# Kernel tuning notes

Hardware: AMD Instinct MI355X
Metric: run time of the kernel (lower is better)

## Reference

```python
import jax, jax.numpy as jnp
import numpy as np

D_MODEL = 2048
NUM_HEADS = 16
N_KV_HEADS = 4
HEAD_DIM = D_MODEL // NUM_HEADS  # 128
N_REP = NUM_HEADS // N_KV_HEADS  # 4
WINDOW = 256
ROPE_BASE = 10000.0
B, T = 2, 2048


def setup_inputs() -> dict:
    key = jax.random.key(0)
    ks = jax.random.split(key, 5)
    s_in = 1.0 / np.sqrt(D_MODEL)
    return {
        "x": jax.random.normal(ks[0], (B, T, D_MODEL), jnp.float32),
        "Wq": jax.random.normal(ks[1], (D_MODEL, D_MODEL), jnp.float32) * s_in,
        "Wk": jax.random.normal(ks[2], (D_MODEL, N_KV_HEADS * HEAD_DIM), jnp.float32) * s_in,
        "Wv": jax.random.normal(ks[3], (D_MODEL, N_KV_HEADS * HEAD_DIM), jnp.float32) * s_in,
        "Wo": jax.random.normal(ks[4], (D_MODEL, D_MODEL), jnp.float32) * s_in,
    }


def _rope_tables(seqlen, dtype):
    inv_freq = 1.0 / (ROPE_BASE ** (jnp.arange(0, HEAD_DIM, 2, dtype=jnp.float32) / HEAD_DIM))
    t = jnp.arange(seqlen, dtype=jnp.float32)
    freqs = jnp.outer(t, inv_freq)              # [T, hd/2]
    emb = jnp.concatenate([freqs, freqs], -1)   # [T, hd]
    return jnp.cos(emb).astype(dtype), jnp.sin(emb).astype(dtype)


def _rotate_half(x):
    half = x.shape[-1] // 2
    return jnp.concatenate([-x[..., half:], x[..., :half]], -1)


def reference(x, Wq, Wk, Wv, Wo):
    Bb, Tt, _ = x.shape
    q = (x @ Wq).reshape(Bb, Tt, NUM_HEADS, HEAD_DIM).transpose(0, 2, 1, 3)   # [B,H,T,hd]
    k = (x @ Wk).reshape(Bb, Tt, N_KV_HEADS, HEAD_DIM).transpose(0, 2, 1, 3)  # [B,Hkv,T,hd]
    v = (x @ Wv).reshape(Bb, Tt, N_KV_HEADS, HEAD_DIM).transpose(0, 2, 1, 3)

    cos, sin = _rope_tables(Tt, q.dtype)  # [T, hd] each, broadcast over B,H
    q = q * cos + _rotate_half(q) * sin
    k = k * cos + _rotate_half(k) * sin

    # GQA: repeat kv heads to match query heads
    k = jnp.repeat(k, N_REP, axis=1)
    v = jnp.repeat(v, N_REP, axis=1)

    # banded causal sliding-window mask: 0 <= i - j < WINDOW
    rel = jnp.arange(Tt)[:, None] - jnp.arange(Tt)[None, :]
    allowed = (rel >= 0) & (rel < WINDOW)  # [T, T]

    scale = 1.0 / np.sqrt(HEAD_DIM)
    scores = jnp.einsum('bhqd,bhkd->bhqk', q, k) * scale
    scores = jnp.where(allowed, scores, jnp.finfo(scores.dtype).min)
    probs = jax.nn.softmax(scores, axis=-1)
    y = jnp.einsum('bhqk,bhkd->bhqd', probs, v)
    y = y.transpose(0, 2, 1, 3).reshape(Bb, Tt, D_MODEL)
    return y @ Wo
```

## Files before the change

### kernel.cpp

```cpp
#include <hip/hip_runtime.h>
#include <hip/hip_bf16.h>

#define D_MODEL 2048
#define SEQ_T   2048
#define NQH     16
#define NKVH    4
#define HD      128
#define WIN     256
#define BATCH   2
#define ROWS    (BATCH * SEQ_T)
#define L2_10K  13.287712379549449f

typedef __attribute__((ext_vector_type(8))) short bf8_t;
typedef __attribute__((ext_vector_type(4))) float f4_t;

__device__ __forceinline__ float bf2f(unsigned short u) {
    union { unsigned int i; float f; } v; v.i = ((unsigned int)u) << 16; return v.f;
}
__device__ __forceinline__ unsigned short f2bf(float f) {
    union { float f; unsigned int i; } v; v.f = f;
    unsigned int x = v.i;
    unsigned int lsb = (x >> 16) & 1u;
    x += 0x7fffu + lsb;
    return (unsigned short)(x >> 16);
}

__device__ __forceinline__ void async_ld16(const unsigned short* g, unsigned short* l) {
    __builtin_amdgcn_global_load_lds(
        (const __attribute__((address_space(1))) unsigned int*)(g),
        (__attribute__((address_space(3))) unsigned int*)(l), 16, 0, 0);
}

__device__ int sniff_is_f32(const unsigned short* p) {
    int sane = 0;
    for (int i = 0; i < 64; ++i) {
        unsigned short u = p[2 * i];
        int e = (u >> 7) & 0xFF;
        sane += (e >= 100 && e <= 140) ? 1 : 0;
    }
    return sane < 32;
}

__global__ __launch_bounds__(256)
void convert_all(const float* __restrict__ x,
                 const float* __restrict__ Wq, const float* __restrict__ Wk,
                 const float* __restrict__ Wv, const float* __restrict__ Wo,
                 unsigned short* __restrict__ xb,
                 unsigned short* __restrict__ Wqkvt, unsigned short* __restrict__ Wot) {
    __shared__ unsigned short Ts[32][36];
    int id = blockIdx.x;
    const int t = threadIdx.x;
    if (id < 4096) {
        int i = (id * 256 + t) * 8;
        float4 a = *(const float4*)(x + i);
        float4 b = *(const float4*)(x + i + 4);
        ushort4 o0, o1;
        o0.x = f2bf(a.x); o0.y = f2bf(a.y); o0.z = f2bf(a.z); o0.w = f2bf(a.w);
        o1.x = f2bf(b.x); o1.y = f2bf(b.y); o1.z = f2bf(b.z); o1.w = f2bf(b.w);
        *(ushort4*)(xb + i)     = o0;
        *(ushort4*)(xb + i + 4) = o1;
        return;
    }
    id -= 4096;
    const float* W; unsigned short* Wt; int N;
    const int K = D_MODEL;
    if (id < 4096)      { W = Wq; Wt = Wqkvt;                          N = 2048; }
    else if (id < 5120) { W = Wk; Wt = Wqkvt + (size_t)2048 * D_MODEL; N = 512;  id -= 4096; }
    else if (id < 6144) { W = Wv; Wt = Wqkvt + (size_t)2560 * D_MODEL; N = 512;  id -= 5120; }
    else                { W = Wo; Wt = Wot;                            N = 2048; id -= 6144; }
    const int ntn = N >> 5;
    const int n0 = (id % ntn) * 32;
    const int k0 = (id / ntn) * 32;
    {
        int r = t >> 3, c = (t & 7) * 4;
        float4 v = *(const float4*)(W + (size_t)(k0 + r) * N + n0 + c);
        Ts[r][c + 0] = f2bf(v.x); Ts[r][c + 1] = f2bf(v.y);
        Ts[r][c + 2] = f2bf(v.z); Ts[r][c + 3] = f2bf(v.w);
    }
    __syncthreads();
    {
        int n = t >> 3, k = (t & 7) * 4;
        ushort4 o;
        o.x = Ts[k + 0][n]; o.y = Ts[k + 1][n];
        o.z = Ts[k + 2][n]; o.w = Ts[k + 3][n];
        *(ushort4*)(Wt + (size_t)(n0 + n) * K + k0 + k) = o;
    }
}

__global__ __launch_bounds__(256)
void gemm_bt128(const unsigned short* __restrict__ A,
                const unsigned short* __restrict__ Bt,
                void* __restrict__ Cq, void* __restrict__ Ck,
                void* __restrict__ Cvc,
                int M, int N, int K, int mode) {
    __shared__ unsigned short As[2][128 * 32];
    __shared__ unsigned short Bs[2][128 * 32];

    const int t    = threadIdx.x;
    const int w    = t >> 6;
    const int lane = t & 63;
    const int quad = lane >> 4;
    const int lr   = lane & 15;
    const int wm   = (w >> 1) * 64;
    const int wnb  = (w & 1);

    const int NX = N >> 7;
    const int TX = NX >> 1;
    const int TYq = (M >> 7) >> 2;
    const int g   = blockIdx.x;
    const int xcd = g & 7;
    const int r   = g >> 3;
    const int bx  = (xcd & 1) * TX + (r % TX);
    const int by  = (xcd >> 1) * TYq + (r / TX);
    const int m0  = by * 128;
    const int n0  = bx * 128;

    const int grow = lane >> 2;
    const int gcol = (lane & 3) * 8;

    f4_t acc[4][4];
    #pragma unroll
    for (int i = 0; i < 4; ++i)
        #pragma unroll
        for (int j = 0; j < 4; ++j)
            acc[i][j] = (f4_t){0.f, 0.f, 0.f, 0.f};

    for (int k0 = 0; k0 < K; k0 += 64) {
        __syncthreads();
        #pragma unroll
        for (int s = 0; s < 2; ++s)
            #pragma unroll
            for (int cc = 0; cc < 2; ++cc) {
                const int c = w + cc * 4;
                async_ld16(A  + (size_t)(m0 + c * 16 + grow) * K + k0 + s * 32 + gcol,
                           &As[s][c * 512]);
                async_ld16(Bt + (size_t)(n0 + c * 16 + grow) * K + k0 + s * 32 + gcol,
                           &Bs[s][c * 512]);
            }
        __syncthreads();

        #pragma unroll
        for (int s = 0; s < 2; ++s) {
            bf8_t af[4], bfr[4];
            #pragma unroll
            for (int i = 0; i < 4; ++i)
                af[i]  = *(const bf8_t*)&As[s][(wm + i * 16 + lr) * 32 + quad * 8];
            #pragma unroll
            for (int j = 0; j < 4; ++j)
                bfr[j] = *(const bf8_t*)&Bs[s][(wnb * 16 + j * 32 + lr) * 32 + quad * 8];
            #pragma unroll
            for (int i = 0; i < 4; ++i)
                #pragma unroll
                for (int j = 0; j < 4; ++j)
                    acc[i][j] = __builtin_amdgcn_mfma_f32_16x16x32_bf16(af[i], bfr[j], acc[i][j], 0, 0, 0);
        }
    }

    if (mode == 1) {
        float* C = (float*)Cq;
        #pragma unroll
        for (int i = 0; i < 4; ++i)
            #pragma unroll
            for (int j = 0; j < 4; ++j) {
                int col = n0 + wnb * 16 + j * 32 + lr;
                #pragma unroll
                for (int rr = 0; rr < 4; ++rr) {
                    int row = m0 + wm + i * 16 + quad * 4 + rr;
                    C[(size_t)row * N + col] = acc[i][j][rr];
                }
            }
    } else {
        if (n0 < 2048 + 512) {
            const bool isQ = (n0 < 2048);
            unsigned short* Cb = isQ ? (unsigned short*)Cq : (unsigned short*)Ck;
            const int ldc   = isQ ? D_MODEL : (NKVH * HD);
            const int cbase = isQ ? n0 : (n0 - 2048);
            float inv[2];
            #pragma unroll
            for (int j = 0; j < 2; ++j) {
                int d = wnb * 16 + j * 32 + lr;
                inv[j] = exp2f(-(float)d * (L2_10K / 64.0f));
            }
            #pragma unroll
            for (int i = 0; i < 4; ++i)
                #pragma unroll
                for (int rr = 0; rr < 4; ++rr) {
                    int row = m0 + wm + i * 16 + quad * 4 + rr;
                    float tp = (float)(row & (SEQ_T - 1));
                    #pragma unroll
                    for (int j = 0; j < 2; ++j) {
                        int d = wnb * 16 + j * 32 + lr;
                        float sn, cs;
                        sincosf(tp * inv[j], &sn, &cs);
                        float lo = acc[i][j][rr], hi = acc[i][j + 2][rr];
                        Cb[(size_t)row * ldc + cbase + d]      = f2bf(lo * cs - hi * sn);
                        Cb[(size_t)row * ldc + cbase + d + 64] = f2bf(hi * cs + lo * sn);
                    }
                }
        } else {
            unsigned short* Vc = (unsigned short*)Cvc;
            #pragma unroll
            for (int i = 0; i < 4; ++i)
                #pragma unroll
                for (int j = 0; j < 4; ++j) {
                    int n    = (n0 - 2560) + wnb * 16 + j * 32 + lr;
                    int kvh2 = n >> 7, d = n & 127;
                    int row0 = m0 + wm + i * 16 + quad * 4;
                    int bb   = row0 >> 11, pos = row0 & (SEQ_T - 1);
                    ushort4 o;
                    o.x = f2bf(acc[i][j][0]); o.y = f2bf(acc[i][j][1]);
                    o.z = f2bf(acc[i][j][2]); o.w = f2bf(acc[i][j][3]);
                    *(ushort4*)(Vc + (size_t)(bb * 4 + kvh2) * (SEQ_T * HD)
                                  + (size_t)(pos >> 5) * 4096 + d * 32 + (pos & 31)) = o;
                }
        }
    }
}

__global__ __launch_bounds__(256)
void gemm_dual(const void* __restrict__ A, const void* __restrict__ B,
               void* __restrict__ C, int M, int N, int Kd,
               const unsigned short* __restrict__ sniffp,
               int a_dyn, int c_dyn, int c_trans) {
    __shared__ unsigned short As[64][32];
    __shared__ unsigned short Bs[64][32];
    __shared__ int s_f32;

    const int t = threadIdx.x;
    if (t == 0) s_f32 = sniff_is_f32(sniffp);

    const int m0 = blockIdx.y * 64, n0 = blockIdx.x * 64;
    const int w = t >> 6, lane = t & 63;
    const int wm = w >> 1, wn = w & 1;
    const int quad = lane >> 4, lr = lane & 15;

    f4_t acc[2][2];
    #pragma unroll
    for (int i = 0; i < 2; ++i)
        #pragma unroll
        for (int j = 0; j < 2; ++j)
            acc[i][j] = (f4_t){0.f, 0.f, 0.f, 0.f};

    const int ar = t >> 2, ac = (t & 3) * 8;
    const int bk = t >> 3, bn = (t & 7) * 8;

    __syncthreads();
    const bool in_f32 = (s_f32 != 0);
    const bool a_f32  = in_f32 && (a_dyn != 0);
    const bool c_f32  = in_f32 && (c_dyn != 0);

    for (int k0 = 0; k0 < Kd; k0 += 32) {
        __syncthreads();
        if (a_f32) {
            const float* Af = (const float*)A;
            const float4* pa = (const float4*)(Af + (size_t)(m0 + ar) * Kd + k0 + ac);
            float4 a0 = pa[0], a1 = pa[1];
            unsigned short* d = &As[ar][ac];
            d[0] = f2bf(a0.x); d[1] = f2bf(a0.y); d[2] = f2bf(a0.z); d[3] = f2bf(a0.w);
            d[4] = f2bf(a1.x); d[5] = f2bf(a1.y); d[6] = f2bf(a1.z); d[7] = f2bf(a1.w);
        } else {
            const unsigned short* Au = (const unsigned short*)A;
            *(uint4*)(&As[ar][ac]) = *(const uint4*)(Au + (size_t)(m0 + ar) * Kd + k0 + ac);
        }
        if (in_f32) {
            const float* Bf = (const float*)B;
            const float4* pb = (const float4*)(Bf + (size_t)(k0 + bk) * N + n0 + bn);
            float4 b0 = pb[0], b1 = pb[1];
            Bs[bn + 0][bk] = f2bf(b0.x); Bs[bn + 1][bk] = f2bf(b0.y);
            Bs[bn + 2][bk] = f2bf(b0.z); Bs[bn + 3][bk] = f2bf(b0.w);
            Bs[bn + 4][bk] = f2bf(b1.x); Bs[bn + 5][bk] = f2bf(b1.y);
            Bs[bn + 6][bk] = f2bf(b1.z); Bs[bn + 7][bk] = f2bf(b1.w);
        } else {
            const unsigned short* Bu = (const unsigned short*)B;
            uint4 bv = *(const uint4*)(Bu + (size_t)(k0 + bk) * N + n0 + bn);
            union { uint4 v; unsigned short s[8]; } bu; bu.v = bv;
            #pragma unroll
            for (int j = 0; j < 8; ++j) Bs[bn + j][bk] = bu.s[j];
        }
        __syncthreads();

        bf8_t va0 = *(const bf8_t*)&As[wm * 32 + 0  + lr][quad * 8];
        bf8_t va1 = *(const bf8_t*)&As[wm * 32 + 16 + lr][quad * 8];
        bf8_t vb0 = *(const bf8_t*)&Bs[wn * 32 + 0  + lr][quad * 8];
        bf8_t vb1 = *(const bf8_t*)&Bs[wn * 32 + 16 + lr][quad * 8];

        acc[0][0] = __builtin_amdgcn_mfma_f32_16x16x32_bf16(va0, vb0, acc[0][0], 0, 0, 0);
        acc[0][1] = __builtin_amdgcn_mfma_f32_16x16x32_bf16(va0, vb1, acc[0][1], 0, 0, 0);
        acc[1][0] = __builtin_amdgcn_mfma_f32_16x16x32_bf16(va1, vb0, acc[1][0], 0, 0, 0);
        acc[1][1] = __builtin_amdgcn_mfma_f32_16x16x32_bf16(va1, vb1, acc[1][1], 0, 0, 0);
    }

    if (c_trans) {
        #pragma unroll
        for (int mi = 0; mi < 2; ++mi)
            #pragma unroll
            for (int ni = 0; ni < 2; ++ni) {
                int row0 = m0 + wm * 32 + mi * 16 + quad * 4;
                int col  = n0 + wn * 32 + ni * 16 + lr;
                int kvh2 = col >> 7, d = col & 127;
                int bb   = row0 >> 11, pos = row0 & (SEQ_T - 1);
                ushort4 v;
                v.x = f2bf(acc[mi][ni][0]); v.y = f2bf(acc[mi][ni][1]);
                v.z = f2bf(acc[mi][ni][2]); v.w = f2bf(acc[mi][ni][3]);
                *(ushort4*)((unsigned short*)C + (size_t)(bb * 4 + kvh2) * (SEQ_T * HD)
                              + (size_t)(pos >> 5) * 4096 + d * 32 + (pos & 31)) = v;
            }
    } else {
        #pragma unroll
        for (int mi = 0; mi < 2; ++mi)
            #pragma unroll
            for (int ni = 0; ni < 2; ++ni)
                #pragma unroll
                for (int r = 0; r < 4; ++r) {
                    int row = m0 + wm * 32 + mi * 16 + quad * 4 + r;
                    int col = n0 + wn * 32 + ni * 16 + lr;
                    if (c_f32) ((float*)C)[(size_t)row * N + col] = acc[mi][ni][r];
                    else ((unsigned short*)C)[(size_t)row * N + col] = f2bf(acc[mi][ni][r]);
                }
    }
}

__global__ __launch_bounds__(64)
void rope_kernel(unsigned short* __restrict__ X, int nheads) {
    const int idx = blockIdx.x;
    const int h   = idx % nheads;
    const int row = idx / nheads;
    const int tpos = row % SEQ_T;
    const int i   = threadIdx.x;

    size_t base = (size_t)row * (nheads * HD) + h * HD;
    float inv = exp2f(-(float)i * (L2_10K / 64.0f));
    float a = (float)tpos * inv;
    float s, c;
    sincosf(a, &s, &c);
    float x0 = bf2f(X[base + i]);
    float x1 = bf2f(X[base + i + 64]);
    X[base + i]      = f2bf(x0 * c - x1 * s);
    X[base + i + 64] = f2bf(x1 * c + x0 * s);
}

#define KSS 136
#define PS  72

__global__ __launch_bounds__(256)
void attn_gqa(unsigned short* __restrict__ Q,
              const unsigned short* __restrict__ K,
              const unsigned short* __restrict__ Vc) {
    __shared__ unsigned short Ks[64][KSS];
    __shared__ unsigned short Vs[8192];
    __shared__ unsigned short Pw[4][32][PS];

    const int t    = threadIdx.x;
    const int g    = blockIdx.x;
    const int xcd  = g & 7;
    const int b    = xcd >> 2;
    const int kvh  = xcd & 3;
    const int q0   = (g >> 3) * 32;
    const int w    = t >> 6;
    const int lane = t & 63;
    const int quad = lane >> 4;
    const int lr   = lane & 15;
    const int h    = kvh * 4 + w;
    const float scale = 0.08838834764831845f;

    bf8_t qf[2][4];
    #pragma unroll
    for (int mt = 0; mt < 2; ++mt) {
        const unsigned short* qrow =
            Q + (size_t)(b * SEQ_T + q0 + mt * 16 + lr) * D_MODEL + h * HD;
        #pragma unroll
        for (int kk = 0; kk < 4; ++kk)
            qf[mt][kk] = *(const bf8_t*)(qrow + kk * 32 + quad * 8);
    }

    f4_t O[2][8];
    #pragma unroll
    for (int mt = 0; mt < 2; ++mt)
        #pragma unroll
        for (int dt = 0; dt < 8; ++dt) O[mt][dt] = (f4_t){0.f, 0.f, 0.f, 0.f};
    float lpart[2][4];
    #pragma unroll
    for (int mt = 0; mt < 2; ++mt)
        #pragma unroll
        for (int r = 0; r < 4; ++r) lpart[mt][r] = 0.f;

    const size_t vbase = (size_t)(b * 4 + kvh) * (SEQ_T * HD);

    for (int j = 0; j < 5; ++j) {
        const int kb = q0 - 256 + 64 * j;
        if (kb + 63 < 0) continue;
        const bool need_mask = (j == 0) || (j == 4) || (kb < 0);

        __syncthreads();
        {
            int row = t >> 2, col = (t & 3) * 32;
            int rg = kb + row;
            rg = rg < 0 ? 0 : (rg > SEQ_T - 1 ? SEQ_T - 1 : rg);
            const unsigned short* src =
                K + (size_t)(b * SEQ_T + rg) * (NKVH * HD) + kvh * HD + col;
            #pragma unroll
            for (int i = 0; i < 4; ++i)
                *(uint4*)&Ks[row][col + 8 * i] = *(const uint4*)(src + 8 * i);
        }
        {
            int s0 = kb >> 5;        s0 = s0 < 0 ? 0 : (s0 > 63 ? 63 : s0);
            int s1 = (kb + 32) >> 5; s1 = s1 < 0 ? 0 : (s1 > 63 ? 63 : s1);
            const unsigned short* vb0 = Vc + vbase + (size_t)s0 * 4096;
            const unsigned short* vb1 = Vc + vbase + (size_t)s1 * 4096;
            #pragma unroll
            for (int i = 0; i < 2; ++i) {
                int off = (w * 2 + i) * 512;
                async_ld16(vb0 + off + lane * 8, &Vs[off]);
                async_ld16(vb1 + off + lane * 8, &Vs[4096 + off]);
            }
        }
        __syncthreads();

        f4_t s[2][4];
        #pragma unroll
        for (int mt = 0; mt < 2; ++mt)
            #pragma unroll
            for (int nt = 0; nt < 4; ++nt) s[mt][nt] = (f4_t){0.f, 0.f, 0.f, 0.f};
        #pragma unroll
        for (int nt = 0; nt < 4; ++nt) {
            #pragma unroll
            for (int kk = 0; kk < 4; ++kk) {
                bf8_t kf = *(const bf8_t*)&Ks[nt * 16 + lr][kk * 32 + quad * 8];
                s[0][nt] = __builtin_amdgcn_mfma_f32_16x16x32_bf16(qf[0][kk], kf, s[0][nt], 0, 0, 0);
                s[1][nt] = __builtin_amdgcn_mfma_f32_16x16x32_bf16(qf[1][kk], kf, s[1][nt], 0, 0, 0);
            }
        }

        #pragma unroll
        for (int mt = 0; mt < 2; ++mt) {
            #pragma unroll
            for (int r = 0; r < 4; ++r) {
                const int q = q0 + mt * 16 + quad * 4 + r;
                #pragma unroll
                for (int nt = 0; nt < 4; ++nt) {
                    float pj = __expf(s[mt][nt][r] * scale);
                    if (need_mask) {
                        int jg = kb + nt * 16 + lr;
                        bool ok = (jg >= 0) && ((unsigned)(q - jg) < (unsigned)WIN);
                        pj = ok ? pj : 0.f;
                    }
                    lpart[mt][r] += pj;
                    Pw[w][mt * 16 + quad * 4 + r][nt * 16 + lr] = f2bf(pj);
                }
            }
        }

        bf8_t pf[2][2];
        #pragma unroll
        for (int mt = 0; mt < 2; ++mt)
            #pragma unroll
            for (int kk = 0; kk < 2; ++kk)
                pf[mt][kk] = *(const bf8_t*)&Pw[w][mt * 16 + lr][kk * 32 + quad * 8];
        #pragma unroll
        for (int dt = 0; dt < 8; ++dt)
            #pragma unroll
            for (int kk = 0; kk < 2; ++kk) {
                bf8_t vf = *(const bf8_t*)&Vs[kk * 4096 + (dt * 16 + lr) * 32 + quad * 8];
                O[0][dt] = __builtin_amdgcn_mfma_f32_16x16x32_bf16(pf[0][kk], vf, O[0][dt], 0, 0, 0);
                O[1][dt] = __builtin_amdgcn_mfma_f32_16x16x32_bf16(pf[1][kk], vf, O[1][dt], 0, 0, 0);
            }
    }

    #pragma unroll
    for (int off = 1; off < 16; off <<= 1)
        #pragma unroll
        for (int mt = 0; mt < 2; ++mt)
            #pragma unroll
            for (int r = 0; r < 4; ++r)
                lpart[mt][r] += __shfl_xor(lpart[mt][r], off);

    #pragma unroll
    for (int mt = 0; mt < 2; ++mt) {
        float invl[4];
        #pragma unroll
        for (int r = 0; r < 4; ++r) invl[r] = 1.0f / lpart[mt][r];
        #pragma unroll
        for (int dt = 0; dt < 8; ++dt)
            #pragma unroll
            for (int r = 0; r < 4; ++r)
                Q[(size_t)(b * SEQ_T + q0 + mt * 16 + quad * 4 + r) * D_MODEL
                  + h * HD + dt * 16 + lr] = f2bf(O[mt][dt][r] * invl[r]);
    }
}

extern "C" void kernel_launch(void* const* d_in, const int* in_sizes, int n_in,
                              void* d_out, int out_size, void* d_ws, size_t ws_size,
                              hipStream_t stream) {
    const float* x  = (const float*)d_in[0];
    const float* Wq = (const float*)d_in[1];
    const float* Wk = (const float*)d_in[2];
    const float* Wv = (const float*)d_in[3];
    const float* Wo = (const float*)d_in[4];
    const unsigned short* sniffp = (const unsigned short*)d_in[1];

    unsigned short* Qb  = (unsigned short*)d_ws;
    unsigned short* Kb  = Qb + (size_t)ROWS * D_MODEL;
    unsigned short* Vcb = Kb + (size_t)ROWS * (NKVH * HD);
    unsigned short* Wot = Vcb + (size_t)(NKVH * HD) * ROWS;

    dim3 blk(256);

    if (ws_size >= (size_t)32 * 1024 * 1024) {
        unsigned short* xb    = (unsigned short*)d_out;
        unsigned short* Wqkvt = xb + (size_t)ROWS * D_MODEL;

        convert_all<<<dim3(14336), blk, 0, stream>>>(x, Wq, Wk, Wv, Wo, xb, Wqkvt, Wot);

        gemm_bt128<<<dim3(768), blk, 0, stream>>>(
            xb, Wqkvt, Qb, Kb, Vcb, ROWS, D_MODEL + 2 * NKVH * HD, D_MODEL, 3);

        attn_gqa<<<dim3(512), blk, 0, stream>>>(Qb, Kb, Vcb);

        gemm_bt128<<<dim3(512), blk, 0, stream>>>(
            Qb, Wot, d_out, nullptr, nullptr, ROWS, D_MODEL, D_MODEL, 1);
    } else {
        gemm_dual<<<dim3(D_MODEL / 64, ROWS / 64), blk, 0, stream>>>(
            x, Wq, Qb, ROWS, D_MODEL, D_MODEL, sniffp, 1, 0, 0);
        gemm_dual<<<dim3((NKVH * HD) / 64, ROWS / 64), blk, 0, stream>>>(
            x, Wk, Kb, ROWS, NKVH * HD, D_MODEL, sniffp, 1, 0, 0);
        gemm_dual<<<dim3((NKVH * HD) / 64, ROWS / 64), blk, 0, stream>>>(
            x, Wv, Vcb, ROWS, NKVH * HD, D_MODEL, sniffp, 1, 0, 1);
        rope_kernel<<<dim3(ROWS * NQH), dim3(64), 0, stream>>>(Qb, NQH);
        rope_kernel<<<dim3(ROWS * NKVH), dim3(64), 0, stream>>>(Kb, NKVH);
        attn_gqa<<<dim3(512), blk, 0, stream>>>(Qb, Kb, Vcb);
        gemm_dual<<<dim3(D_MODEL / 64, ROWS / 64), blk, 0, stream>>>(
            Qb, Wo, d_out, ROWS, D_MODEL, D_MODEL, sniffp, 0, 1, 0);
    }
}
```

Baseline: 272.6 us.

## Replace 128x128 GEMM with 256x256 tile, 4-stage async LDS pipeline

Replaces the 128x128 double-buffered GEMM with a 512-thread 256x256 tile kernel. It uses a 4-deep ring of async global-to-LDS loads gated by vmcnt waits and a single barrier per k-step, a swizzled LDS layout to avoid bank conflicts, and s_setprio around the MFMA bursts. The larger tile raises data reuse per load and the deeper pipeline hides memory latency. In exchange, grid size falls to 192 and 128 blocks on a 256-CU part, so many CUs sit idle and wave quantization gets worse. The kernel also hardcodes K=2048 and a specific tile-to-XCD mapping.

Result: faster. 252.1 us (-7.5%).

```diff
diff --git a/kernel.cpp b/kernel.cpp
--- a/kernel.cpp
+++ b/kernel.cpp
@@ -10,6 +10,8 @@
 #define BATCH   2
 #define ROWS    (BATCH * SEQ_T)
 #define L2_10K  13.287712379549449f
+#define GK      2048
+#define GNT     64
 
 typedef __attribute__((ext_vector_type(8))) short bf8_t;
 typedef __attribute__((ext_vector_type(4))) float f4_t;
@@ -87,133 +89,152 @@
     }
 }
 
-__global__ __launch_bounds__(256)
-void gemm_bt128(const unsigned short* __restrict__ A,
-                const unsigned short* __restrict__ Bt,
-                void* __restrict__ Cq, void* __restrict__ Ck,
-                void* __restrict__ Cvc,
-                int M, int N, int K, int mode) {
-    __shared__ unsigned short As[2][128 * 32];
-    __shared__ unsigned short Bs[2][128 * 32];
-
-    const int t    = threadIdx.x;
-    const int w    = t >> 6;
-    const int lane = t & 63;
+__global__ __launch_bounds__(512, 2)
+void gemm256(const unsigned short* __restrict__ A,
+             const unsigned short* __restrict__ Bt,
+             void* __restrict__ Cq, void* __restrict__ Ck, void* __restrict__ Cvc,
+             int N, int mode) {
+    __shared__ __align__(16) unsigned short Ls[4][2][8192];
+
+    const int tid  = threadIdx.x;
+    const int w    = tid >> 6;
+    const int lane = tid & 63;
     const int quad = lane >> 4;
     const int lr   = lane & 15;
-    const int wm   = (w >> 1) * 64;
-    const int wnb  = (w & 1);
-
-    const int NX = N >> 7;
-    const int TX = NX >> 1;
-    const int TYq = (M >> 7) >> 2;
+    const int wm   = w >> 2;
+    const int wn   = w & 3;
+    const int sl   = ((quad + (lr >> 1)) & 3) * 8;
+
+    const int ntn = N >> 8;
     const int g   = blockIdx.x;
     const int xcd = g & 7;
     const int r   = g >> 3;
-    const int bx  = (xcd & 1) * TX + (r % TX);
-    const int by  = (xcd >> 1) * TYq + (r / TX);
-    const int m0  = by * 128;
-    const int n0  = bx * 128;
-
-    const int grow = lane >> 2;
-    const int gcol = (lane & 3) * 8;
-
-    f4_t acc[4][4];
-    #pragma unroll
-    for (int i = 0; i < 4; ++i)
-        #pragma unroll
-        for (int j = 0; j < 4; ++j)
-            acc[i][j] = (f4_t){0.f, 0.f, 0.f, 0.f};
-
-    for (int k0 = 0; k0 < K; k0 += 64) {
-        __syncthreads();
-        #pragma unroll
-        for (int s = 0; s < 2; ++s)
-            #pragma unroll
-            for (int cc = 0; cc < 2; ++cc) {
-                const int c = w + cc * 4;
-                async_ld16(A  + (size_t)(m0 + c * 16 + grow) * K + k0 + s * 32 + gcol,
-                           &As[s][c * 512]);
-                async_ld16(Bt + (size_t)(n0 + c * 16 + grow) * K + k0 + s * 32 + gcol,
-                           &Bs[s][c * 512]);
-            }
-        __syncthreads();
-
-        #pragma unroll
-        for (int s = 0; s < 2; ++s) {
-            bf8_t af[4], bfr[4];
-            #pragma unroll
-            for (int i = 0; i < 4; ++i)
-                af[i]  = *(const bf8_t*)&As[s][(wm + i * 16 + lr) * 32 + quad * 8];
-            #pragma unroll
-            for (int j = 0; j < 4; ++j)
-                bfr[j] = *(const bf8_t*)&Bs[s][(wnb * 16 + j * 32 + lr) * 32 + quad * 8];
-            #pragma unroll
-            for (int i = 0; i < 4; ++i)
-                #pragma unroll
-                for (int j = 0; j < 4; ++j)
-                    acc[i][j] = __builtin_amdgcn_mfma_f32_16x16x32_bf16(af[i], bfr[j], acc[i][j], 0, 0, 0);
-        }
-    }
+    const int bm  = (xcd & 3) * 4 + (r & 3);
+    const int bn  = (xcd >> 2) * (ntn >> 1) + (r >> 2);
+    const int m0  = bm * 256;
+    const int n0  = bn * 256;
+
+    const unsigned short* srcA[2];
+    const unsigned short* srcB[2];
+    int dchunk[2];
+    #pragma unroll
+    for (int l = 0; l < 2; ++l) {
+        int li   = l * 512 + tid;
+        int row  = li >> 2;
+        int slog = ((li & 3) - ((li >> 3) & 3)) & 3;
+        srcA[l]   = A  + (size_t)(m0 + row) * GK + slog * 8;
+        srcB[l]   = Bt + (size_t)(n0 + row) * GK + slog * 8;
+        dchunk[l] = (l * 512 + w * 64) * 8;
+    }
+
+    f4_t acc[8][4];
+    #pragma unroll
+    for (int i = 0; i < 8; ++i)
+        #pragma unroll
+        for (int j = 0; j < 4; ++j) acc[i][j] = (f4_t){0.f, 0.f, 0.f, 0.f};
+
+#define STAGE(S, KT) do {                                           \
+        const int ko_ = (KT) * 32;                                  \
+        async_ld16(srcA[0] + ko_, &Ls[S][0][dchunk[0]]);            \
+        async_ld16(srcA[1] + ko_, &Ls[S][0][dchunk[1]]);            \
+        async_ld16(srcB[0] + ko_, &Ls[S][1][dchunk[0]]);            \
+        async_ld16(srcB[1] + ko_, &Ls[S][1][dchunk[1]]);            \
+    } while (0)
+
+#define TILE(S) do {                                                          \
+        const unsigned short* LA_ = &Ls[S][0][0];                             \
+        const unsigned short* LB_ = &Ls[S][1][0];                             \
+        bf8_t af[8], bv[4];                                                   \
+        _Pragma("unroll")                                                     \
+        for (int mf = 0; mf < 8; ++mf)                                        \
+            af[mf] = *(const bf8_t*)&LA_[(wm * 128 + mf * 16 + lr) * 32 + sl];\
+        _Pragma("unroll")                                                     \
+        for (int nf = 0; nf < 4; ++nf)                                        \
+            bv[nf] = *(const bf8_t*)&LB_[(wn * 16 + nf * 64 + lr) * 32 + sl]; \
+        __builtin_amdgcn_s_setprio(1);                                        \
+        _Pragma("unroll")                                                     \
+        for (int nf = 0; nf < 4; ++nf)                                        \
+            _Pragma("unroll")                                                 \
+            for (int mf = 0; mf < 8; ++mf)                                    \
+                acc[mf][nf] = __builtin_amdgcn_mfma_f32_16x16x32_bf16(        \
+                    af[mf], bv[nf], acc[mf][nf], 0, 0, 0);                    \
+        __builtin_amdgcn_s_setprio(0);                                        \
+    } while (0)
+
+#define GATE(NN) asm volatile("s_waitcnt vmcnt(" #NN ")" ::: "memory")
+
+    STAGE(0, 0); STAGE(1, 1); STAGE(2, 2);
+    GATE(8);
+    __builtin_amdgcn_s_barrier();
+
+    for (int t = 0; t < 61; ++t) {
+        STAGE((t + 3) & 3, t + 3);
+        TILE(t & 3);
+        GATE(8);
+        __builtin_amdgcn_s_barrier();
+    }
+    TILE(1); GATE(4); __builtin_amdgcn_s_barrier();
+    TILE(2); GATE(0); __builtin_amdgcn_s_barrier();
+    TILE(3);
+
+#undef STAGE
+#undef TILE
+#undef GATE
 
     if (mode == 1) {
         float* C = (float*)Cq;
         #pragma unroll
-        for (int i = 0; i < 4; ++i)
-            #pragma unroll
-            for (int j = 0; j < 4; ++j) {
-                int col = n0 + wnb * 16 + j * 32 + lr;
+        for (int mf = 0; mf < 8; ++mf)
+            #pragma unroll
+            for (int nf = 0; nf < 4; ++nf) {
+                int c  = n0 + wn * 16 + nf * 64 + lr;
+                int rb = m0 + wm * 128 + mf * 16 + quad * 4;
                 #pragma unroll
-                for (int rr = 0; rr < 4; ++rr) {
-                    int row = m0 + wm + i * 16 + quad * 4 + rr;
-                    C[(size_t)row * N + col] = acc[i][j][rr];
+                for (int rr = 0; rr < 4; ++rr)
+                    C[(size_t)(rb + rr) * N + c] = acc[mf][nf][rr];
+            }
+        return;
+    }
+    if (n0 < 2048 + 512) {
+        const bool isQ = (n0 < 2048);
+        unsigned short* Cb = isQ ? (unsigned short*)Cq : (unsigned short*)Ck;
+        const int ldc = isQ ? D_MODEL : (NKVH * HD);
+        const int cb0 = isQ ? n0 : (n0 - 2048);
+        const int dh  = wn * 16 + lr;
+        const float inv = exp2f(-(float)dh * (L2_10K / 64.0f));
+        #pragma unroll
+        for (int mf = 0; mf < 8; ++mf) {
+            #pragma unroll
+            for (int rr = 0; rr < 4; ++rr) {
+                int row = m0 + wm * 128 + mf * 16 + quad * 4 + rr;
+                float tp = (float)(row & (SEQ_T - 1));
+                float sn, cs;
+                sincosf(tp * inv, &sn, &cs);
+                #pragma unroll
+                for (int p = 0; p < 2; ++p) {
+                    float lo = acc[mf][2 * p][rr], hi = acc[mf][2 * p + 1][rr];
+                    size_t base = (size_t)row * ldc + cb0 + wn * 16 + p * 128 + lr;
+                    Cb[base]      = f2bf(lo * cs - hi * sn);
+                    Cb[base + 64] = f2bf(hi * cs + lo * sn);
                 }
             }
+        }
     } else {
-        if (n0 < 2048 + 512) {
-            const bool isQ = (n0 < 2048);
-            unsigned short* Cb = isQ ? (unsigned short*)Cq : (unsigned short*)Ck;
-            const int ldc   = isQ ? D_MODEL : (NKVH * HD);
-            const int cbase = isQ ? n0 : (n0 - 2048);
-            float inv[2];
-            #pragma unroll
-            for (int j = 0; j < 2; ++j) {
-                int d = wnb * 16 + j * 32 + lr;
-                inv[j] = exp2f(-(float)d * (L2_10K / 64.0f));
-            }
-            #pragma unroll
-            for (int i = 0; i < 4; ++i)
-                #pragma unroll
-                for (int rr = 0; rr < 4; ++rr) {
-                    int row = m0 + wm + i * 16 + quad * 4 + rr;
-                    float tp = (float)(row & (SEQ_T - 1));
-                    #pragma unroll
-                    for (int j = 0; j < 2; ++j) {
-                        int d = wnb * 16 + j * 32 + lr;
-                        float sn, cs;
-                        sincosf(tp * inv[j], &sn, &cs);
-                        float lo = acc[i][j][rr], hi = acc[i][j + 2][rr];
-                        Cb[(size_t)row * ldc + cbase + d]      = f2bf(lo * cs - hi * sn);
-                        Cb[(size_t)row * ldc + cbase + d + 64] = f2bf(hi * cs + lo * sn);
-                    }
-                }
-        } else {
-            unsigned short* Vc = (unsigned short*)Cvc;
-            #pragma unroll
-            for (int i = 0; i < 4; ++i)
-                #pragma unroll
-                for (int j = 0; j < 4; ++j) {
-                    int n    = (n0 - 2560) + wnb * 16 + j * 32 + lr;
-                    int kvh2 = n >> 7, d = n & 127;
-                    int row0 = m0 + wm + i * 16 + quad * 4;
-                    int bb   = row0 >> 11, pos = row0 & (SEQ_T - 1);
-                    ushort4 o;
-                    o.x = f2bf(acc[i][j][0]); o.y = f2bf(acc[i][j][1]);
-                    o.z = f2bf(acc[i][j][2]); o.w = f2bf(acc[i][j][3]);
-                    *(ushort4*)(Vc + (size_t)(bb * 4 + kvh2) * (SEQ_T * HD)
-                                  + (size_t)(pos >> 5) * 4096 + d * 32 + (pos & 31)) = o;
-                }
-        }
+        unsigned short* Vc = (unsigned short*)Cvc;
+        #pragma unroll
+        for (int mf = 0; mf < 8; ++mf)
+            #pragma unroll
+            for (int nf = 0; nf < 4; ++nf) {
+                int n    = (n0 - 2560) + wn * 16 + nf * 64 + lr;
+                int kvh2 = n >> 7, d = n & 127;
+                int row0 = m0 + wm * 128 + mf * 16 + quad * 4;
+                int bb   = row0 >> 11, pos = row0 & (SEQ_T - 1);
+                ushort4 o;
+                o.x = f2bf(acc[mf][nf][0]); o.y = f2bf(acc[mf][nf][1]);
+                o.z = f2bf(acc[mf][nf][2]); o.w = f2bf(acc[mf][nf][3]);
+                *(ushort4*)(Vc + (size_t)(bb * 4 + kvh2) * (SEQ_T * HD)
+                              + (size_t)(pos >> 5) * 4096 + d * 32 + (pos & 31)) = o;
+            }
     }
 }
 
@@ -511,13 +532,13 @@
 
         convert_all<<<dim3(14336), blk, 0, stream>>>(x, Wq, Wk, Wv, Wo, xb, Wqkvt, Wot);
 
-        gemm_bt128<<<dim3(768), blk, 0, stream>>>(
-            xb, Wqkvt, Qb, Kb, Vcb, ROWS, D_MODEL + 2 * NKVH * HD, D_MODEL, 3);
+        gemm256<<<dim3(192), dim3(512), 0, stream>>>(
+            xb, Wqkvt, Qb, Kb, Vcb, D_MODEL + 2 * NKVH * HD, 3);
 
         attn_gqa<<<dim3(512), blk, 0, stream>>>(Qb, Kb, Vcb);
 
-        gemm_bt128<<<dim3(512), blk, 0, stream>>>(
-            Qb, Wot, d_out, nullptr, nullptr, ROWS, D_MODEL, D_MODEL, 1);
+        gemm256<<<dim3(128), dim3(512), 0, stream>>>(
+            Qb, Wot, d_out, nullptr, nullptr, D_MODEL, 1);
     } else {
         gemm_dual<<<dim3(D_MODEL / 64, ROWS / 64), blk, 0, stream>>>(
             x, Wq, Qb, ROWS, D_MODEL, D_MODEL, sniffp, 1, 0, 0);
```
